# Performance work log

Hardware: AMD Instinct MI355X
Metric: run time of the kernel (lower is better)

## Reference

```python
import jax, jax.numpy as jnp
import numpy as np

N_NODES = 50000
EPS = 1e-12  # F.normalize eps


def _gcn_layer(x, W, b, src, dst):
    # GCNConv(normalize=False): h = x @ W, then sum-aggregate messages from
    # source nodes into target nodes along edge_index, then add bias.
    h = x @ W
    agg = jax.ops.segment_sum(h[src], dst, num_segments=N_NODES)
    out = agg + b
    # F.normalize(p=2, dim=-1) then ReLU
    norm = jnp.linalg.norm(out, axis=-1, keepdims=True)
    out = out / jnp.maximum(norm, EPS)
    return jax.nn.relu(out)


def setup_inputs() -> dict:
    key = jax.random.key(0)
    ks = jax.random.split(key, 8)
    nfeat, nhid, nclass, n_edges = 128, 128, 40, 640000
    x = jax.random.normal(ks[0], (N_NODES, nfeat), dtype=jnp.float32)
    edge_index = jax.random.randint(ks[1], (2, n_edges), 0, N_NODES, dtype=jnp.int64)
    s = 1.0 / np.sqrt(nhid)
    return {
        "x": x,
        "edge_index": edge_index,
        "W1": jax.random.normal(ks[2], (nfeat, nhid), jnp.float32) * s,
        "b1": jnp.zeros((nhid,), jnp.float32),
        "W2": jax.random.normal(ks[3], (nhid, nhid), jnp.float32) * s,
        "b2": jnp.zeros((nhid,), jnp.float32),
        "W3": jax.random.normal(ks[4], (nhid, nhid), jnp.float32) * s,
        "b3": jnp.zeros((nhid,), jnp.float32),
        "W4": jax.random.normal(ks[5], (nhid, nhid), jnp.float32) * s,
        "b4": jnp.zeros((nhid,), jnp.float32),
        "Wl": jax.random.normal(ks[6], (nhid, nclass), jnp.float32) * s,
        "bl": jnp.zeros((nclass,), jnp.float32),
    }


def reference(x, edge_index, W1, b1, W2, b2, W3, b3, W4, b4, Wl, bl):
    src, dst = edge_index[0], edge_index[1]
    x1 = _gcn_layer(x, W1, b1, src, dst)
    x2 = _gcn_layer(x1, W2, b2, src, dst)
    x3 = _gcn_layer(x2, W3, b3, src, dst)
    x4 = _gcn_layer(x3, W4, b4, src, dst)
    logits = x4 @ Wl + bl
    probs = jax.nn.softmax(logits, axis=-1)
    return (logits, probs, x4)
```

## Files before the change

kernel.cpp:

```cpp
#include <hip/hip_runtime.h>
#include <hip/hip_bf16.h>
#include <hip/hip_fp16.h>
#include <math.h>

#define NFEAT 128
#define NCLASS 40

typedef __attribute__((ext_vector_type(8))) short frag_ab;
typedef __attribute__((ext_vector_type(4))) float frag_cd;

static __device__ inline unsigned short f2bf_rne(float f) {
    union { float f; unsigned u; } v;
    v.f = f;
    unsigned r = v.u + 0x7FFFu + ((v.u >> 16) & 1u);
    return (unsigned short)(r >> 16);
}
static __device__ inline float bf2f(unsigned short h) {
    union { unsigned u; float f; } v;
    v.u = ((unsigned)h) << 16;
    return v.f;
}


__global__ __launch_bounds__(256) void prep_kernel(const float* __restrict__ x,
                                                   __half* __restrict__ xh, int xc4,
                                                   const float* __restrict__ W0,
                                                   const float* __restrict__ W1,
                                                   const float* __restrict__ W2,
                                                   const float* __restrict__ W3,
                                                   short* __restrict__ whi,
                                                   short* __restrict__ wlo,
                                                   const int* __restrict__ dst,
                                                   int* __restrict__ cnt, int n_edges,
                                                   int convB) {
    int b = blockIdx.x;
    if (b < convB) {
        int i = b * 256 + threadIdx.x;
        if (i < xc4) {
            float4 v = ((const float4*)x)[i];
            ((__half2*)xh)[i * 2 + 0] = __floats2half2_rn(v.x, v.y);
            ((__half2*)xh)[i * 2 + 1] = __floats2half2_rn(v.z, v.w);
        }
    } else if (b < convB + 32) {
        int wb = b - convB;
        int layer = wb >> 3;
        const float* W = layer == 0 ? W0 : layer == 1 ? W1 : layer == 2 ? W2 : W3;
        short* h = whi + (size_t)layer * 16384;
        short* l = wlo + (size_t)layer * 16384;
        int idx = (wb & 7) * 256 + threadIdx.x;
        int lane = idx & 63;
        int t = (idx >> 6) & 7;
        int s = idx >> 9;
        int quad = lane >> 4;
        int n = lane & 15;
        int kbase = s * 32 + quad * 8;
        int col = t * 16 + n;
#pragma unroll
        for (int j = 0; j < 8; ++j) {
            float f = W[(size_t)(kbase + j) * NFEAT + col];
            unsigned short hb = f2bf_rne(f);
            unsigned short lb = f2bf_rne(f - bf2f(hb));
            h[(size_t)idx * 8 + j] = (short)hb;
            l[(size_t)idx * 8 + j] = (short)lb;
        }
    } else {
        int hb = b - convB - 32;
        int i = hb * 256 + threadIdx.x;
        int n4 = n_edges >> 2;
        if (i < n4) {
            int4 d = ((const int4*)dst)[i];
            atomicAdd(&cnt[d.x], 1);
            atomicAdd(&cnt[d.y], 1);
            atomicAdd(&cnt[d.z], 1);
            atomicAdd(&cnt[d.w], 1);
        }
        if (hb == 0 && threadIdx.x == 0) {
            for (int e = n4 << 2; e < n_edges; ++e) atomicAdd(&cnt[dst[e]], 1);
        }
    }
}


__global__ __launch_bounds__(256) void scan1_kernel(const int* __restrict__ cnt,
                                                    int* __restrict__ excl,
                                                    int* __restrict__ bsums, int n) {
    __shared__ int sd[256];
    int t = threadIdx.x;
    int i = blockIdx.x * 256 + t;
    int v = (i < n) ? cnt[i] : 0;
    sd[t] = v;
    __syncthreads();
#pragma unroll
    for (int off = 1; off < 256; off <<= 1) {
        int tmp = (t >= off) ? sd[t - off] : 0;
        __syncthreads();
        sd[t] += tmp;
        __syncthreads();
    }
    if (i < n) excl[i] = sd[t] - v;
    if (t == 255) bsums[blockIdx.x] = sd[255];
}

__global__ __launch_bounds__(256) void scan3_kernel(const int* __restrict__ excl,
                                                    const int* __restrict__ bsums,
                                                    int* __restrict__ row_ptr,
                                                    int* __restrict__ woff, int n, int nb) {
    __shared__ int sd[256];
    __shared__ int off_s, tot_s;
    int t = threadIdx.x;
    int v = (t < nb) ? bsums[t] : 0;
    sd[t] = v;
    __syncthreads();
#pragma unroll
    for (int off = 1; off < 256; off <<= 1) {
        int tmp = (t >= off) ? sd[t - off] : 0;
        __syncthreads();
        sd[t] += tmp;
        __syncthreads();
    }
    if (t == 0) {
        off_s = (blockIdx.x > 0) ? sd[blockIdx.x - 1] : 0;
        tot_s = sd[255];
    }
    __syncthreads();
    int i = blockIdx.x * 256 + t;
    if (i < n) {
        int val = excl[i] + off_s;
        row_ptr[i] = val;
        woff[i] = val;
    }
    if (i == 0) row_ptr[n] = tot_s;
}

__global__ __launch_bounds__(256) void scatter_kernel(const int* __restrict__ src,
                                                      const int* __restrict__ dst,
                                                      int* __restrict__ woff,
                                                      int* __restrict__ src_sorted, int n_edges) {
    int i = blockIdx.x * 256 + threadIdx.x;
    int n4 = n_edges >> 2;
    if (i < n4) {
        int4 d = ((const int4*)dst)[i];
        int4 s = ((const int4*)src)[i];
        int p0 = atomicAdd(&woff[d.x], 1);
        int p1 = atomicAdd(&woff[d.y], 1);
        int p2 = atomicAdd(&woff[d.z], 1);
        int p3 = atomicAdd(&woff[d.w], 1);
        src_sorted[p0] = s.x;
        src_sorted[p1] = s.y;
        src_sorted[p2] = s.z;
        src_sorted[p3] = s.w;
    }
    if (i == 0) {
        for (int e = n4 << 2; e < n_edges; ++e) {
            int p = atomicAdd(&woff[dst[e]], 1);
            src_sorted[p] = src[e];
        }
    }
}


__global__ __launch_bounds__(256) void gcn_fused_kernel(const __half* __restrict__ xin,
                                                        const int* __restrict__ row_ptr,
                                                        const int* __restrict__ src_sorted,
                                                        const short* __restrict__ whi,
                                                        const short* __restrict__ wlo,
                                                        const float* __restrict__ bias,
                                                        float* __restrict__ outf,
                                                        __half* __restrict__ outh, int M) {
    __shared__ float smem[64][132];
    __shared__ int ctr;
    int tid = threadIdx.x;
    int base = blockIdx.x * 64;
    if (tid == 0) ctr = 0;
    __syncthreads();

    {
        int c = tid & 15;
        int lane = tid & 63;
        const uint4* xp = (const uint4*)xin;
        for (;;) {
            int nl = 0;
            if ((lane & 15) == 0) nl = atomicAdd(&ctr, 1);
            nl = __shfl(nl, lane & 48);
            if (nl >= 64) break;
            int node = base + nl;
            float a[8];
#pragma unroll
            for (int i = 0; i < 8; ++i) a[i] = 0.f;
            int jb = 0, je = 0;
            if (node < M) { jb = row_ptr[node]; je = row_ptr[node + 1]; }

            int j = jb;
            int i0 = 0, i1 = 0, i2 = 0, i3 = 0;
            bool have4 = (j + 4 <= je);
            if (have4) {
                i0 = src_sorted[j];
                i1 = src_sorted[j + 1];
                i2 = src_sorted[j + 2];
                i3 = src_sorted[j + 3];
            }
            while (have4) {
                uint4 r0 = xp[i0 * 16 + c];
                uint4 r1 = xp[i1 * 16 + c];
                uint4 r2 = xp[i2 * 16 + c];
                uint4 r3 = xp[i3 * 16 + c];
                int jn = j + 4;
                bool more = (jn + 4 <= je);
                if (more) {
                    i0 = src_sorted[jn];
                    i1 = src_sorted[jn + 1];
                    i2 = src_sorted[jn + 2];
                    i3 = src_sorted[jn + 3];
                }
#pragma unroll
                for (int q = 0; q < 4; ++q) {
                    unsigned u0 = (&r0.x)[q], u1 = (&r1.x)[q], u2 = (&r2.x)[q], u3 = (&r3.x)[q];
                    float2 f0 = __half22float2(*(__half2*)&u0);
                    float2 f1 = __half22float2(*(__half2*)&u1);
                    float2 f2 = __half22float2(*(__half2*)&u2);
                    float2 f3 = __half22float2(*(__half2*)&u3);
                    a[q * 2 + 0] += f0.x + f1.x + f2.x + f3.x;
                    a[q * 2 + 1] += f0.y + f1.y + f2.y + f3.y;
                }
                j = jn;
                have4 = more;
            }
            for (; j < je; ++j) {
                int s0 = src_sorted[j];
                uint4 r0 = xp[s0 * 16 + c];
#pragma unroll
                for (int q = 0; q < 4; ++q) {
                    unsigned u0 = (&r0.x)[q];
                    float2 f0 = __half22float2(*(__half2*)&u0);
                    a[q * 2 + 0] += f0.x;
                    a[q * 2 + 1] += f0.y;
                }
            }
            float4* wp = (float4*)&smem[nl][c * 8];
            wp[0] = make_float4(a[0], a[1], a[2], a[3]);
            wp[1] = make_float4(a[4], a[5], a[6], a[7]);
        }
    }
    __syncthreads();

    int wave = tid >> 6;
    int lane = tid & 63;
    int quad = lane >> 4;
    int n16 = lane & 15;
    int lrow = wave * 16 + n16;

    const frag_ab* WH = (const frag_ab*)whi;
    const frag_ab* WL = (const frag_ab*)wlo;

    frag_cd acc[8];
#pragma unroll
    for (int t = 0; t < 8; ++t) acc[t] = (frag_cd){0.f, 0.f, 0.f, 0.f};

#pragma unroll
    for (int s = 0; s < 4; ++s) {
        const float* ap = &smem[lrow][s * 32 + quad * 8];
        float4 v0 = *(const float4*)(ap);
        float4 v1 = *(const float4*)(ap + 4);
        float fv[8] = {v0.x, v0.y, v0.z, v0.w, v1.x, v1.y, v1.z, v1.w};
        frag_ab ah, al;
#pragma unroll
        for (int jj = 0; jj < 8; ++jj) {
            unsigned short hb = f2bf_rne(fv[jj]);
            ah[jj] = (short)hb;
            al[jj] = (short)f2bf_rne(fv[jj] - bf2f(hb));
        }
#pragma unroll
        for (int t = 0; t < 8; ++t) {
            frag_ab bh = WH[(s * 8 + t) * 64 + lane];
            frag_ab bl = WL[(s * 8 + t) * 64 + lane];
            acc[t] = __builtin_amdgcn_mfma_f32_16x16x32_bf16(ah, bh, acc[t], 0, 0, 0);
            acc[t] = __builtin_amdgcn_mfma_f32_16x16x32_bf16(ah, bl, acc[t], 0, 0, 0);
            acc[t] = __builtin_amdgcn_mfma_f32_16x16x32_bf16(al, bh, acc[t], 0, 0, 0);
        }
    }

    float ssq[4] = {0.f, 0.f, 0.f, 0.f};
#pragma unroll
    for (int t = 0; t < 8; ++t) {
        float bv = bias[t * 16 + n16];
#pragma unroll
        for (int r = 0; r < 4; ++r) {
            acc[t][r] += bv;
            ssq[r] += acc[t][r] * acc[t][r];
        }
    }
#pragma unroll
    for (int mask = 1; mask <= 8; mask <<= 1) {
#pragma unroll
        for (int r = 0; r < 4; ++r) ssq[r] += __shfl_xor(ssq[r], mask);
    }
    float inv[4];
#pragma unroll
    for (int r = 0; r < 4; ++r) inv[r] = 1.0f / fmaxf(sqrtf(ssq[r]), 1e-12f);

    int orow0 = base + wave * 16 + quad * 4;
#pragma unroll
    for (int r = 0; r < 4; ++r) {
        int orow = orow0 + r;
        if (orow < M) {
            if (outh) {
                __half* op = outh + (size_t)orow * NFEAT + n16;
#pragma unroll
                for (int t = 0; t < 8; ++t)
                    op[t * 16] = __float2half(fmaxf(acc[t][r] * inv[r], 0.f));
            } else {
                float* op = outf + (size_t)orow * NFEAT + n16;
#pragma unroll
                for (int t = 0; t < 8; ++t)
                    op[t * 16] = fmaxf(acc[t][r] * inv[r], 0.f);
            }
        }
    }
}


__global__ __launch_bounds__(256) void classifier_kernel(const float* __restrict__ x4,
                                                         const float* __restrict__ Wl,
                                                         const float* __restrict__ bl,
                                                         float* __restrict__ logits,
                                                         float* __restrict__ probs, int n_nodes) {
    int node = blockIdx.x * 256 + threadIdx.x;
    int nc = node < n_nodes ? node : n_nodes - 1;
    const float* row = x4 + (size_t)nc * NFEAT;

    float acc[NCLASS];
#pragma unroll
    for (int c = 0; c < NCLASS; ++c) acc[c] = bl[c];

    for (int k = 0; k < NFEAT; k += 4) {
        float4 a = *(const float4*)(row + k);
#pragma unroll
        for (int kk = 0; kk < 4; ++kk) {
            float av = (&a.x)[kk];
            const float* Wr = Wl + (k + kk) * NCLASS;
#pragma unroll
            for (int c = 0; c < NCLASS; ++c) acc[c] += av * Wr[c];
        }
    }

    float m = acc[0];
#pragma unroll
    for (int c = 1; c < NCLASS; ++c) m = fmaxf(m, acc[c]);
    float ex[NCLASS];
    float sum = 0.f;
#pragma unroll
    for (int c = 0; c < NCLASS; ++c) {
        ex[c] = __expf(acc[c] - m);
        sum += ex[c];
    }
    float is = 1.0f / sum;

    if (node < n_nodes) {
        float4* lo = (float4*)(logits + (size_t)node * NCLASS);
        float4* po = (float4*)(probs + (size_t)node * NCLASS);
#pragma unroll
        for (int c = 0; c < NCLASS; c += 4) {
            float4 lv, pv;
            lv.x = acc[c + 0]; lv.y = acc[c + 1]; lv.z = acc[c + 2]; lv.w = acc[c + 3];
            pv.x = ex[c + 0] * is; pv.y = ex[c + 1] * is; pv.z = ex[c + 2] * is; pv.w = ex[c + 3] * is;
            lo[c >> 2] = lv;
            po[c >> 2] = pv;
        }
    }
}


extern "C" void kernel_launch(void* const* d_in, const int* in_sizes, int n_in,
                              void* d_out, int out_size, void* d_ws, size_t ws_size,
                              hipStream_t stream) {
    const float* x  = (const float*)d_in[0];
    const int*   ei = (const int*)d_in[1];
    const float* W1 = (const float*)d_in[2];
    const float* b1 = (const float*)d_in[3];
    const float* W2 = (const float*)d_in[4];
    const float* b2 = (const float*)d_in[5];
    const float* W3 = (const float*)d_in[6];
    const float* b3 = (const float*)d_in[7];
    const float* W4 = (const float*)d_in[8];
    const float* b4 = (const float*)d_in[9];
    const float* Wl = (const float*)d_in[10];
    const float* bl = (const float*)d_in[11];

    const int n_nodes = in_sizes[0] / NFEAT;
    const int n_edges = in_sizes[1] / 2;
    const int* src = ei;
    const int* dst = ei + n_edges;

    float* out    = (float*)d_out;
    float* logits = out;
    float* probs  = out + (size_t)n_nodes * NCLASS;
    float* x4     = out + 2 * (size_t)n_nodes * NCLASS;

    char* ws = (char*)d_ws;
    size_t off = 0;
    auto wsalloc = [&](size_t bytes) -> void* {
        void* p = ws + off;
        off += (bytes + 255) & ~(size_t)255;
        return p;
    };
    __half* xh         = (__half*)wsalloc((size_t)n_nodes * NFEAT * sizeof(__half));
    __half* xh2        = (__half*)wsalloc((size_t)n_nodes * NFEAT * sizeof(__half));
    int*    row_ptr    = (int*)wsalloc(((size_t)n_nodes + 1) * sizeof(int));
    int*    woff       = (int*)wsalloc((size_t)n_nodes * sizeof(int));
    int*    cnt        = (int*)wsalloc((size_t)n_nodes * sizeof(int));
    int*    src_sorted = (int*)wsalloc((size_t)n_edges * sizeof(int));
    int     nbt        = (n_nodes + 255) / 256;
    int*    bsums      = (int*)wsalloc(((size_t)nbt + 1) * sizeof(int));
    short*  whi        = (short*)wsalloc((size_t)4 * 16384 * sizeof(short));
    short*  wlo        = (short*)wsalloc((size_t)4 * 16384 * sizeof(short));

    hipMemsetAsync(cnt, 0, (size_t)n_nodes * sizeof(int), stream);

    int xc4   = (n_nodes * NFEAT) / 4;
    int convB = (xc4 + 255) / 256;
    int e4b   = ((n_edges >> 2) + 255) / 256;
    prep_kernel<<<convB + 32 + e4b, 256, 0, stream>>>(x, xh, xc4,
                                                      W1, W2, W3, W4, whi, wlo,
                                                      dst, cnt, n_edges, convB);

    scan1_kernel<<<nbt, 256, 0, stream>>>(cnt, row_ptr , bsums, n_nodes);
    scan3_kernel<<<nbt, 256, 0, stream>>>(row_ptr, bsums, row_ptr, woff, n_nodes, nbt);
    scatter_kernel<<<e4b, 256, 0, stream>>>(src, dst, woff, src_sorted, n_edges);

    int gb = (n_nodes + 63) / 64;
    int cb = (n_nodes + 255) / 256;

    gcn_fused_kernel<<<gb, 256, 0, stream>>>(xh,  row_ptr, src_sorted, whi + 0 * 16384, wlo + 0 * 16384, b1, nullptr, xh2, n_nodes);
    gcn_fused_kernel<<<gb, 256, 0, stream>>>(xh2, row_ptr, src_sorted, whi + 1 * 16384, wlo + 1 * 16384, b2, nullptr, xh,  n_nodes);
    gcn_fused_kernel<<<gb, 256, 0, stream>>>(xh,  row_ptr, src_sorted, whi + 2 * 16384, wlo + 2 * 16384, b3, nullptr, xh2, n_nodes);
    gcn_fused_kernel<<<gb, 256, 0, stream>>>(xh2, row_ptr, src_sorted, whi + 3 * 16384, wlo + 3 * 16384, b4, x4, nullptr, n_nodes);

    classifier_kernel<<<cb, 256, 0, stream>>>(x4, Wl, bl, logits, probs, n_nodes);
}
```

Baseline: 350.3 us.

## Sort nodes by in-degree into a permutation for load-balanced GCN blocks

Builds a degree histogram during the scan and a counting-sort permutation that groups nodes with similar in-degree (descending) into the same 64-node block. The fused GCN kernel processes nodes via this permutation and writes outputs back to the original rows. The aim is to even out per-block gather work and get the heavy blocks scheduled first, which should cut tail imbalance. In exchange it adds an indirection, scattered output writes, and extra atomics and a serial 64-entry prefix per scan block.

```diff
diff --git a/kernel.cpp b/kernel.cpp
--- a/kernel.cpp
+++ b/kernel.cpp
@@ -83,10 +83,13 @@
 
 __global__ __launch_bounds__(256) void scan1_kernel(const int* __restrict__ cnt,
                                                     int* __restrict__ excl,
-                                                    int* __restrict__ bsums, int n) {
+                                                    int* __restrict__ bsums,
+                                                    int* __restrict__ hist, int n) {
     __shared__ int sd[256];
+    __shared__ int lh[64];
     int t = threadIdx.x;
     int i = blockIdx.x * 256 + t;
+    if (t < 64) lh[t] = 0;
     int v = (i < n) ? cnt[i] : 0;
     sd[t] = v;
     __syncthreads();
@@ -97,17 +100,31 @@
         sd[t] += tmp;
         __syncthreads();
     }
-    if (i < n) excl[i] = sd[t] - v;
+    if (i < n) {
+        excl[i] = sd[t] - v;
+        atomicAdd(&lh[v < 63 ? v : 63], 1);
+    }
     if (t == 255) bsums[blockIdx.x] = sd[255];
+    __syncthreads();
+    if (t < 64 && lh[t]) atomicAdd(&hist[t], lh[t]);
 }
 
 __global__ __launch_bounds__(256) void scan3_kernel(const int* __restrict__ excl,
                                                     const int* __restrict__ bsums,
                                                     int* __restrict__ row_ptr,
-                                                    int* __restrict__ woff, int n, int nb) {
+                                                    int* __restrict__ woff,
+                                                    const int* __restrict__ cnt,
+                                                    const int* __restrict__ hist,
+                                                    int* __restrict__ hoff,
+                                                    int* __restrict__ perm,
+                                                    int n, int nb) {
     __shared__ int sd[256];
     __shared__ int off_s, tot_s;
+    __shared__ int hincl[64];
+    __shared__ int bcnt[64];
+    __shared__ int bbase[64];
     int t = threadIdx.x;
+    if (t < 64) bcnt[t] = 0;
     int v = (t < nb) ? bsums[t] : 0;
     sd[t] = v;
     __syncthreads();
@@ -121,15 +138,27 @@
     if (t == 0) {
         off_s = (blockIdx.x > 0) ? sd[blockIdx.x - 1] : 0;
         tot_s = sd[255];
+        int s = 0;
+        for (int d = 0; d < 64; ++d) { s += hist[d]; hincl[d] = s; }
     }
     __syncthreads();
     int i = blockIdx.x * 256 + t;
+    int d = 0, myslot = 0;
     if (i < n) {
         int val = excl[i] + off_s;
         row_ptr[i] = val;
         woff[i] = val;
+        int deg = cnt[i];
+        d = deg < 63 ? deg : 63;
+        myslot = atomicAdd(&bcnt[d], 1);
     }
     if (i == 0) row_ptr[n] = tot_s;
+    __syncthreads();
+    if (t < 64 && bcnt[t]) bbase[t] = atomicAdd(&hoff[t], bcnt[t]);
+    __syncthreads();
+    if (i < n) {
+        perm[(n - hincl[d]) + bbase[d] + myslot] = i;
+    }
 }
 
 __global__ __launch_bounds__(256) void scatter_kernel(const int* __restrict__ src,
@@ -162,6 +191,7 @@
 __global__ __launch_bounds__(256) void gcn_fused_kernel(const __half* __restrict__ xin,
                                                         const int* __restrict__ row_ptr,
                                                         const int* __restrict__ src_sorted,
+                                                        const int* __restrict__ perm,
                                                         const short* __restrict__ whi,
                                                         const short* __restrict__ wlo,
                                                         const float* __restrict__ bias,
@@ -183,12 +213,16 @@
             if ((lane & 15) == 0) nl = atomicAdd(&ctr, 1);
             nl = __shfl(nl, lane & 48);
             if (nl >= 64) break;
-            int node = base + nl;
+            int slot = base + nl;
             float a[8];
 #pragma unroll
             for (int i = 0; i < 8; ++i) a[i] = 0.f;
             int jb = 0, je = 0;
-            if (node < M) { jb = row_ptr[node]; je = row_ptr[node + 1]; }
+            if (slot < M) {
+                int node = perm[slot];
+                jb = row_ptr[node];
+                je = row_ptr[node + 1];
+            }
 
             int j = jb;
             int i0 = 0, i1 = 0, i2 = 0, i3 = 0;
@@ -298,11 +332,12 @@
 #pragma unroll
     for (int r = 0; r < 4; ++r) inv[r] = 1.0f / fmaxf(sqrtf(ssq[r]), 1e-12f);
 
-    int orow0 = base + wave * 16 + quad * 4;
+    int slot0 = base + wave * 16 + quad * 4;
 #pragma unroll
     for (int r = 0; r < 4; ++r) {
-        int orow = orow0 + r;
-        if (orow < M) {
+        int slot = slot0 + r;
+        if (slot < M) {
+            int orow = perm[slot];
             if (outh) {
                 __half* op = outh + (size_t)orow * NFEAT + n16;
 #pragma unroll
@@ -407,14 +442,17 @@
     __half* xh2        = (__half*)wsalloc((size_t)n_nodes * NFEAT * sizeof(__half));
     int*    row_ptr    = (int*)wsalloc(((size_t)n_nodes + 1) * sizeof(int));
     int*    woff       = (int*)wsalloc((size_t)n_nodes * sizeof(int));
-    int*    cnt        = (int*)wsalloc((size_t)n_nodes * sizeof(int));
+    int*    cnt        = (int*)wsalloc(((size_t)n_nodes + 128) * sizeof(int));
+    int*    hist       = cnt + n_nodes;
+    int*    hoff       = cnt + n_nodes + 64;
+    int*    perm       = (int*)wsalloc((size_t)n_nodes * sizeof(int));
     int*    src_sorted = (int*)wsalloc((size_t)n_edges * sizeof(int));
     int     nbt        = (n_nodes + 255) / 256;
     int*    bsums      = (int*)wsalloc(((size_t)nbt + 1) * sizeof(int));
     short*  whi        = (short*)wsalloc((size_t)4 * 16384 * sizeof(short));
     short*  wlo        = (short*)wsalloc((size_t)4 * 16384 * sizeof(short));
 
-    hipMemsetAsync(cnt, 0, (size_t)n_nodes * sizeof(int), stream);
+    hipMemsetAsync(cnt, 0, ((size_t)n_nodes + 128) * sizeof(int), stream);
 
     int xc4   = (n_nodes * NFEAT) / 4;
     int convB = (xc4 + 255) / 256;
@@ -423,17 +461,18 @@
                                                       W1, W2, W3, W4, whi, wlo,
                                                       dst, cnt, n_edges, convB);
 
-    scan1_kernel<<<nbt, 256, 0, stream>>>(cnt, row_ptr , bsums, n_nodes);
-    scan3_kernel<<<nbt, 256, 0, stream>>>(row_ptr, bsums, row_ptr, woff, n_nodes, nbt);
+    scan1_kernel<<<nbt, 256, 0, stream>>>(cnt, row_ptr , bsums, hist, n_nodes);
+    scan3_kernel<<<nbt, 256, 0, stream>>>(row_ptr, bsums, row_ptr, woff,
+                                          cnt, hist, hoff, perm, n_nodes, nbt);
     scatter_kernel<<<e4b, 256, 0, stream>>>(src, dst, woff, src_sorted, n_edges);
 
     int gb = (n_nodes + 63) / 64;
     int cb = (n_nodes + 255) / 256;
 
-    gcn_fused_kernel<<<gb, 256, 0, stream>>>(xh,  row_ptr, src_sorted, whi + 0 * 16384, wlo + 0 * 16384, b1, nullptr, xh2, n_nodes);
-    gcn_fused_kernel<<<gb, 256, 0, stream>>>(xh2, row_ptr, src_sorted, whi + 1 * 16384, wlo + 1 * 16384, b2, nullptr, xh,  n_nodes);
-    gcn_fused_kernel<<<gb, 256, 0, stream>>>(xh,  row_ptr, src_sorted, whi + 2 * 16384, wlo + 2 * 16384, b3, nullptr, xh2, n_nodes);
-    gcn_fused_kernel<<<gb, 256, 0, stream>>>(xh2, row_ptr, src_sorted, whi + 3 * 16384, wlo + 3 * 16384, b4, x4, nullptr, n_nodes);
+    gcn_fused_kernel<<<gb, 256, 0, stream>>>(xh,  row_ptr, src_sorted, perm, whi + 0 * 16384, wlo + 0 * 16384, b1, nullptr, xh2, n_nodes);
+    gcn_fused_kernel<<<gb, 256, 0, stream>>>(xh2, row_ptr, src_sorted, perm, whi + 1 * 16384, wlo + 1 * 16384, b2, nullptr, xh,  n_nodes);
+    gcn_fused_kernel<<<gb, 256, 0, stream>>>(xh,  row_ptr, src_sorted, perm, whi + 2 * 16384, wlo + 2 * 16384, b3, nullptr, xh2, n_nodes);
+    gcn_fused_kernel<<<gb, 256, 0, stream>>>(xh2, row_ptr, src_sorted, perm, whi + 3 * 16384, wlo + 3 * 16384, b4, x4, nullptr, n_nodes);
 
     classifier_kernel<<<cb, 256, 0, stream>>>(x4, Wl, bl, logits, probs, n_nodes);
 }
```

Measured after the change: 348.8 us. About the same (-0.5%).
